# Optimization experiments

Hardware: AMD Instinct MI355X
Metric: run time of the kernel (lower is better)

## Reference

```python
import jax, jax.numpy as jnp
import numpy as np

B, VS, VO = 16, 10475, 8192
K, PS, PO = 64, 1024, 2048


def setup_inputs() -> dict:
    key = jax.random.key(0)
    k1, k2, k3, k4, k5 = jax.random.split(key, 5)
    smplx_v = jax.random.normal(k1, (B, VS, 3), dtype=jnp.float32)
    object_v = jax.random.normal(k2, (B, VO, 3), dtype=jnp.float32)
    smpl_part_idx = jax.random.randint(k3, (K, PS), 0, VS, dtype=jnp.int64) if jax.config.jax_enable_x64 else jax.random.randint(k3, (K, PS), 0, VS, dtype=jnp.int32)
    obj_part_idx = jax.random.randint(k4, (K, PO), 0, VO, dtype=jnp.int32)
    batch_idx = jax.random.randint(k5, (K,), 0, B, dtype=jnp.int32)
    return {
        'smplx_v': smplx_v,
        'object_v': object_v,
        'smpl_part_idx': smpl_part_idx,
        'obj_part_idx': obj_part_idx,
        'batch_idx': batch_idx,
    }


def reference(smplx_v, object_v, smpl_part_idx, obj_part_idx, batch_idx):
    # Batched gather of per-pair contact vertex subsets.
    sc = smplx_v[batch_idx[:, None], smpl_part_idx]   # [K, PS, 3]
    oc = object_v[batch_idx[:, None], obj_part_idx]   # [K, PO, 3]
    # Pairwise Euclidean distances [K, PS, PO] (torch.norm of differences).
    diff = sc[:, :, None, :] - oc[:, None, :, :]
    d = jnp.sqrt(jnp.sum(diff * diff, axis=-1))
    # One-directional chamfer: min over object verts, mean over smpl verts,
    # then mean over all contact pairs (torch.stack(...).mean()).
    loss = jnp.mean(jnp.mean(jnp.min(d, axis=-1), axis=-1))
    return loss
```

## Files before the change

### kernel.cpp

```cpp
#include <hip/hip_runtime.h>
#include <float.h>
#include <math.h>

constexpr int B  = 16;
constexpr int VS = 10475;
constexpr int VO = 8192;
constexpr int K  = 64;
constexpr int PS = 1024;
constexpr int PO = 2048;

constexpr int BLK  = 1024;
constexpr int QPB  = 256;
constexpr int GRID = K * (PS / QPB);
constexpr int NW   = 16;
constexpr int NT   = PO / 16;

typedef float  v3f  __attribute__((ext_vector_type(3)));
typedef float  f32x4 __attribute__((ext_vector_type(4)));
typedef _Float16 half8 __attribute__((ext_vector_type(8)));
typedef unsigned int u32;
typedef u32 v4u  __attribute__((ext_vector_type(4)));

__device__ __forceinline__ u32 pkh(_Float16 lo, _Float16 hi) {
    const unsigned short l = __builtin_bit_cast(unsigned short, lo);
    const unsigned short h = __builtin_bit_cast(unsigned short, hi);
    return ((u32)h << 16) | (u32)l;
}


__global__ __launch_bounds__(BLK)
void cl_onepass(const float* __restrict__ smplx_v,
                const float* __restrict__ object_v,
                const int*   __restrict__ spi,
                const int*   __restrict__ opi,
                const int*   __restrict__ bidx,
                float*       __restrict__ partial)
{
    __shared__ u32   so[(PO + 16) * 4];
    __shared__ float wsum[NW];

    const int bk   = blockIdx.x;
    const int tid  = threadIdx.x;
    const int k    = bk >> 2;
    const int ic   = bk & 3;
    const int b    = bidx[k];
    const int wave = tid >> 6;
    const int lane = tid & 63;

    const float* __restrict__ ov = object_v + (size_t)b * VO * 3;
    #pragma unroll
    for (int r = 0; r < PO / BLK; ++r) {
        const int j  = r * BLK + tid;
        const int oj = opi[k * PO + j];
        const v3f p  = *(const v3f*)(ov + 3 * (size_t)oj);
        const _Float16 hx = (_Float16)p.x, hy = (_Float16)p.y, hz = (_Float16)p.z;
        const float fx = (float)hx, fy = (float)hy, fz = (float)hz;
        const float w2 = 0.5f * (fx * fx + fy * fy + fz * fz);
        const _Float16 w2h = (_Float16)w2;
        const _Float16 w2l = (_Float16)(w2 - (float)w2h);
        const u32 d0 = pkh(hx, hy);
        *(v4u*)&so[j * 4] = (v4u){d0, pkh(hz, w2h), d0, pkh(hz, w2l)};
    }
    if (tid < 64) so[PO * 4 + tid] = 0;

    half8 afrag = (half8)(_Float16)0;
    float s2 = 0.0f;
    if (lane < 16) {
        const int i  = ic * QPB + wave * 16 + lane;
        const int si = spi[k * PS + i];
        const v3f s  = *(const v3f*)(smplx_v + 3 * ((size_t)b * VS + si));
        s2 = s.x * s.x + s.y * s.y + s.z * s.z;
        const _Float16 shx = (_Float16)s.x, shy = (_Float16)s.y, shz = (_Float16)s.z;
        const _Float16 slx = (_Float16)(s.x - (float)shx);
        const _Float16 sly = (_Float16)(s.y - (float)shy);
        const _Float16 slz = (_Float16)(s.z - (float)shz);
        const _Float16 n1  = (_Float16)(-1.0f);
        afrag = (half8){shx, shy, shz, n1, slx, sly, slz, n1};
    }
    __syncthreads();

    const u32* bp = (lane < 16) ? &so[lane * 4]
                                : &so[PO * 4 + (lane & 15) * 4];
    const int  inc = (lane < 16) ? 64 : 0;

    f32x4 mint = (f32x4){FLT_MAX, FLT_MAX, FLT_MAX, FLT_MAX};
    #pragma unroll 8
    for (int t = 0; t < NT; ++t) {
        const half8 bfrag = *(const half8*)bp;
        const f32x4 d = __builtin_amdgcn_mfma_f32_16x16x32_f16(
            afrag, bfrag, (f32x4){0.f, 0.f, 0.f, 0.f}, 0, 0, 0);
        mint.x = fminf(mint.x, -d.x);
        mint.y = fminf(mint.y, -d.y);
        mint.z = fminf(mint.z, -d.z);
        mint.w = fminf(mint.w, -d.w);
        bp += inc;
    }

    #pragma unroll
    for (int m = 1; m <= 8; m <<= 1) {
        mint.x = fminf(mint.x, __shfl_xor(mint.x, m, 64));
        mint.y = fminf(mint.y, __shfl_xor(mint.y, m, 64));
        mint.z = fminf(mint.z, __shfl_xor(mint.z, m, 64));
        mint.w = fminf(mint.w, __shfl_xor(mint.w, m, 64));
    }

    const int src = (lane >> 2) << 4;
    const float t0 = __shfl(mint.x, src, 64);
    const float t1 = __shfl(mint.y, src, 64);
    const float t2 = __shfl(mint.z, src, 64);
    const float t3 = __shfl(mint.w, src, 64);
    const int rsel = lane & 3;
    const float tmy = (rsel == 0) ? t0 : (rsel == 1) ? t1 : (rsel == 2) ? t2 : t3;

    float d = 0.0f;
    if (lane < 16)
        d = sqrtf(fmaxf(fmaf(2.0f, tmy, s2), 0.0f));

    #pragma unroll
    for (int m = 1; m <= 8; m <<= 1)
        d += __shfl_xor(d, m, 64);
    if (lane == 0) wsum[wave] = d;
    __syncthreads();

    if (tid < 64) {
        float v = (tid < NW) ? wsum[tid] : 0.0f;
        #pragma unroll
        for (int off = 8; off > 0; off >>= 1)
            v += __shfl_down(v, off, 64);
        if (tid == 0) partial[bk] = v;
    }
}


__global__ __launch_bounds__(64)
void cl_final(const float* __restrict__ partial, float* __restrict__ out)
{
    const int t = threadIdx.x;
    const float4 a = ((const float4*)partial)[t];
    float v = (a.x + a.y) + (a.z + a.w);
    #pragma unroll
    for (int off = 32; off > 0; off >>= 1)
        v += __shfl_down(v, off, 64);
    if (t == 0) out[0] = v * (1.0f / (float)(K * PS));
}


extern "C" void kernel_launch(void* const* d_in, const int* in_sizes, int n_in,
                              void* d_out, int out_size, void* d_ws, size_t ws_size,
                              hipStream_t stream)
{
    const float* smplx_v       = (const float*)d_in[0];
    const float* object_v      = (const float*)d_in[1];
    const int*   smpl_part_idx = (const int*)d_in[2];
    const int*   obj_part_idx  = (const int*)d_in[3];
    const int*   batch_idx     = (const int*)d_in[4];
    float*       out           = (float*)d_out;

    float* partial = (float*)d_ws;

    cl_onepass<<<GRID, BLK, 0, stream>>>(
        smplx_v, object_v, smpl_part_idx, obj_part_idx, batch_idx, partial);
    cl_final<<<1, 64, 0, stream>>>(partial, out);
}
```

Measured before the change: 16.51 us.

## Switch to 32x32x16 MFMA with object-half split across waves

Replaces the 16x16x32 MFMA tile with a 32x32x16 one. Each wave now handles 32 query points against half of the object points, and the two halves are min-combined through shared memory. The 32x32 tile makes each LDS B-fragment load feed more outputs and halves the number of MFMA issues per wave. In exchange it adds an extra LDS reduction and barrier, and each lane keeps 16 accumulators live for the running minimum, which raises register pressure.

```diff
diff --git a/kernel.cpp b/kernel.cpp
--- a/kernel.cpp
+++ b/kernel.cpp
@@ -9,17 +9,18 @@
 constexpr int PS = 1024;
 constexpr int PO = 2048;
 
-constexpr int BLK  = 1024;
-constexpr int QPB  = 256;
-constexpr int GRID = K * (PS / QPB);
-constexpr int NW   = 16;
-constexpr int NT   = PO / 16;
+constexpr int BLK   = 1024;
+constexpr int QPB   = 256;
+constexpr int GRID  = K * (PS / QPB);
+constexpr int NW    = 16;
+constexpr int OHALF = PO / 2;
+constexpr int NT    = OHALF / 32;
 
-typedef float  v3f  __attribute__((ext_vector_type(3)));
-typedef float  f32x4 __attribute__((ext_vector_type(4)));
+typedef float  v3f    __attribute__((ext_vector_type(3)));
+typedef float  f32x16 __attribute__((ext_vector_type(16)));
 typedef _Float16 half8 __attribute__((ext_vector_type(8)));
 typedef unsigned int u32;
-typedef u32 v4u  __attribute__((ext_vector_type(4)));
+typedef u32 v4u __attribute__((ext_vector_type(4)));
 
 __device__ __forceinline__ u32 pkh(_Float16 lo, _Float16 hi) {
     const unsigned short l = __builtin_bit_cast(unsigned short, lo);
@@ -37,7 +38,9 @@
                 float*       __restrict__ partial)
 {
     __shared__ u32   so[(PO + 16) * 4];
-    __shared__ float wsum[NW];
+    __shared__ float red[NW][32];
+    __shared__ float s2lds[QPB];
+    __shared__ float wsum[4];
 
     const int bk   = blockIdx.x;
     const int tid  = threadIdx.x;
@@ -46,6 +49,8 @@
     const int b    = bidx[k];
     const int wave = tid >> 6;
     const int lane = tid & 63;
+    const int qg   = wave & 7;
+    const int oh   = wave >> 3;
 
     const float* __restrict__ ov = object_v + (size_t)b * VO * 3;
     #pragma unroll
@@ -64,71 +69,71 @@
     if (tid < 64) so[PO * 4 + tid] = 0;
 
     half8 afrag = (half8)(_Float16)0;
-    float s2 = 0.0f;
-    if (lane < 16) {
-        const int i  = ic * QPB + wave * 16 + lane;
+    if (lane < 32) {
+        const int i  = ic * QPB + qg * 32 + lane;
         const int si = spi[k * PS + i];
         const v3f s  = *(const v3f*)(smplx_v + 3 * ((size_t)b * VS + si));
-        s2 = s.x * s.x + s.y * s.y + s.z * s.z;
+        const float s2 = s.x * s.x + s.y * s.y + s.z * s.z;
         const _Float16 shx = (_Float16)s.x, shy = (_Float16)s.y, shz = (_Float16)s.z;
         const _Float16 slx = (_Float16)(s.x - (float)shx);
         const _Float16 sly = (_Float16)(s.y - (float)shy);
         const _Float16 slz = (_Float16)(s.z - (float)shz);
         const _Float16 n1  = (_Float16)(-1.0f);
         afrag = (half8){shx, shy, shz, n1, slx, sly, slz, n1};
+        if (wave < 8) s2lds[qg * 32 + lane] = s2;
     }
     __syncthreads();
 
-    const u32* bp = (lane < 16) ? &so[lane * 4]
-                                : &so[PO * 4 + (lane & 15) * 4];
-    const int  inc = (lane < 16) ? 64 : 0;
+    const u32* bp  = (lane < 32) ? &so[((size_t)oh * OHALF + (lane & 31)) * 4]
+                                 : &so[PO * 4];
+    const int  inc = (lane < 32) ? 32 * 4 : 0;
 
-    f32x4 mint = (f32x4){FLT_MAX, FLT_MAX, FLT_MAX, FLT_MAX};
-    #pragma unroll 8
+    f32x16 mint;
+    #pragma unroll
+    for (int i = 0; i < 16; ++i) mint[i] = FLT_MAX;
+
+    #pragma unroll 4
     for (int t = 0; t < NT; ++t) {
         const half8 bfrag = *(const half8*)bp;
-        const f32x4 d = __builtin_amdgcn_mfma_f32_16x16x32_f16(
-            afrag, bfrag, (f32x4){0.f, 0.f, 0.f, 0.f}, 0, 0, 0);
-        mint.x = fminf(mint.x, -d.x);
-        mint.y = fminf(mint.y, -d.y);
-        mint.z = fminf(mint.z, -d.z);
-        mint.w = fminf(mint.w, -d.w);
+        f32x16 zc;
+        #pragma unroll
+        for (int i = 0; i < 16; ++i) zc[i] = 0.0f;
+        const f32x16 d = __builtin_amdgcn_mfma_f32_32x32x16_f16(
+            afrag, bfrag, zc, 0, 0, 0);
+        #pragma unroll
+        for (int i = 0; i < 16; ++i) mint[i] = fminf(mint[i], -d[i]);
         bp += inc;
     }
 
     #pragma unroll
-    for (int m = 1; m <= 8; m <<= 1) {
-        mint.x = fminf(mint.x, __shfl_xor(mint.x, m, 64));
-        mint.y = fminf(mint.y, __shfl_xor(mint.y, m, 64));
-        mint.z = fminf(mint.z, __shfl_xor(mint.z, m, 64));
-        mint.w = fminf(mint.w, __shfl_xor(mint.w, m, 64));
+    for (int m = 1; m <= 16; m <<= 1) {
+        #pragma unroll
+        for (int i = 0; i < 16; ++i)
+            mint[i] = fminf(mint[i], __shfl_xor(mint[i], m, 64));
     }
 
-    const int src = (lane >> 2) << 4;
-    const float t0 = __shfl(mint.x, src, 64);
-    const float t1 = __shfl(mint.y, src, 64);
-    const float t2 = __shfl(mint.z, src, 64);
-    const float t3 = __shfl(mint.w, src, 64);
-    const int rsel = lane & 3;
-    const float tmy = (rsel == 0) ? t0 : (rsel == 1) ? t1 : (rsel == 2) ? t2 : t3;
+    if ((lane & 31) == 0) {
+        const int h = lane >> 5;
+        #pragma unroll
+        for (int reg = 0; reg < 16; ++reg) {
+            const int row = (reg & 3) + 8 * (reg >> 2) + 4 * h;
+            red[wave][row] = mint[reg];
+        }
+    }
+    __syncthreads();
 
     float d = 0.0f;
-    if (lane < 16)
-        d = sqrtf(fmaxf(fmaf(2.0f, tmy, s2), 0.0f));
-
+    if (tid < QPB) {
+        const int q2 = tid >> 5, row = tid & 31;
+        const float m = fminf(red[q2][row], red[q2 + 8][row]);
+        d = sqrtf(fmaxf(fmaf(2.0f, m, s2lds[tid]), 0.0f));
+    }
     #pragma unroll
-    for (int m = 1; m <= 8; m <<= 1)
-        d += __shfl_xor(d, m, 64);
-    if (lane == 0) wsum[wave] = d;
+    for (int off = 32; off > 0; off >>= 1)
+        d += __shfl_down(d, off, 64);
+    if (lane == 0 && wave < 4) wsum[wave] = d;
     __syncthreads();
-
-    if (tid < 64) {
-        float v = (tid < NW) ? wsum[tid] : 0.0f;
-        #pragma unroll
-        for (int off = 8; off > 0; off >>= 1)
-            v += __shfl_down(v, off, 64);
-        if (tid == 0) partial[bk] = v;
-    }
+    if (tid == 0) partial[bk] = (wsum[0] + wsum[1]) + (wsum[2] + wsum[3]);
 }
 
 
```

Measured after the change: 16.59 us. Within noise of the previous version (+0.5%).
